# Optimization experiments

Hardware: AMD Instinct MI355X
Metric: run time of the kernel (lower is better)

Reference implementation:

```python
import jax, jax.numpy as jnp
import numpy as np
from math import factorial

N_NODES = 10000
N_EDGES = 320000
FEAT = 32
NBASIS = 8
RMAX = 6.0
ZMAX = 119


def _cg(j1, m1, j2, m2, j3, m3):
    if m1 + m2 != m3 or j3 < abs(j1 - j2) or j3 > j1 + j2:
        return 0.0
    f = lambda n: float(factorial(n))
    pre = ((2 * j3 + 1) * f(j1 + j2 - j3) * f(j1 - j2 + j3) * f(-j1 + j2 + j3) / f(j1 + j2 + j3 + 1)) ** 0.5
    pre *= (f(j3 + m3) * f(j3 - m3) * f(j1 - m1) * f(j1 + m1) * f(j2 - m2) * f(j2 + m2)) ** 0.5
    s = 0.0
    for k in range(j1 + j2 + j3 + 1):
        d = [k, j1 + j2 - j3 - k, j1 - m1 - k, j2 + m2 - k, j3 - j2 + m1 + k, j3 - j1 - m2 + k]
        if min(d) < 0:
            continue
        s += (-1) ** k / (f(d[0]) * f(d[1]) * f(d[2]) * f(d[3]) * f(d[4]) * f(d[5]))
    return pre * s


def _u_real(l):
    # complex->real spherical harmonics unitary transform
    U = np.zeros((2 * l + 1, 2 * l + 1), dtype=complex)
    s2 = 1.0 / np.sqrt(2.0)
    for m in range(-l, l + 1):
        i = m + l
        if m == 0:
            U[i, l] = 1.0
        elif m > 0:
            U[i, l + m] = ((-1) ** m) * s2
            U[i, l - m] = s2
        else:
            U[i, l + m] = 1j * s2
            U[i, l - m] = -1j * ((-1) ** m) * s2
    return U


def _real_cg():
    # real Clebsch-Gordan coupling coefficients for l<=2, shape (9,9,9), sparse
    off = [0, 1, 4]
    C = np.zeros((9, 9, 9))
    Us = [_u_real(l) for l in range(3)]
    for l1 in range(3):
        for l2 in range(3):
            for l3 in range(3):
                if l3 < abs(l1 - l2) or l3 > l1 + l2:
                    continue
                cg = np.zeros((2 * l1 + 1, 2 * l2 + 1, 2 * l3 + 1))
                for m1 in range(-l1, l1 + 1):
                    for m2 in range(-l2, l2 + 1):
                        m3 = m1 + m2
                        if abs(m3) <= l3:
                            cg[m1 + l1, m2 + l2, m3 + l3] = _cg(l1, m1, l2, m2, l3, m3)
                blk = np.einsum('ia,jb,kc,abc->ijk', Us[l1], Us[l2], np.conj(Us[l3]), cg.astype(complex))
                C[off[l1]:off[l1] + 2 * l1 + 1, off[l2]:off[l2] + 2 * l2 + 1, off[l3]:off[l3] + 2 * l3 + 1] = blk.real + blk.imag
    return C

CGC = jnp.asarray(_real_cg(), dtype=jnp.float32)
SL = [slice(0, 1), slice(1, 4), slice(4, 9)]
PATHS0 = [(0, 0, 0), (0, 1, 1), (0, 2, 2)]
PATHS1 = [(l1, l2, l3) for l1 in range(3) for l2 in range(3) for l3 in range(3) if abs(l1 - l2) <= l3 <= l1 + l2]
PATHS2 = [(0, 0, 0), (1, 1, 0), (2, 2, 0)]


def _real_sph(u):
    x, y, z = u[:, 0], u[:, 1], u[:, 2]
    c0 = 0.28209479177387814
    c1 = 0.4886025119029199
    c2a = 1.0925484305920792
    c2b = 0.31539156525252005
    c2c = 0.5462742152960396
    return jnp.stack([c0 * jnp.ones_like(x), c1 * y, c1 * z, c1 * x,
                      c2a * x * y, c2a * y * z, c2b * (3.0 * z * z - 1.0), c2a * x * z,
                      c2c * (x * x - y * y)], axis=-1)


def _message_pass(x, rad, Y, src, dst, W, paths, out_dim, n_nodes):
    # gather src node features -> per-edge CG tensor product with (radial x Ylm) basis -> scatter-add to dst
    xs = x[src, 0]  # (E, Dx, F)
    msg = jnp.zeros((rad.shape[0], out_dim, x.shape[-1]), x.dtype)
    for p, (l1, l2, l3) in enumerate(paths):
        w = rad @ W[p]  # (E, F) learned radial path weights
        contrib = jnp.einsum('abc,eaf,eb,ef->ecf', CGC[SL[l1], SL[l2], SL[l3]], xs[:, SL[l1], :], Y[:, SL[l2]], w)
        msg = msg.at[:, SL[l3], :].add(contrib)
    y = jax.ops.segment_sum(msg, dst, num_segments=n_nodes)
    return y[:, None]  # (N, 1, out_dim, F)


def _eadd(a, b):
    if a.shape[2] == b.shape[2]:
        return a + b
    if a.shape[2] < b.shape[2]:
        a, b = b, a
    return a.at[:, :, :b.shape[2], :].add(b)


def _edense(x, K, b):
    # equivariant Dense: shared kernel across degrees, bias only on scalar (l=0) channel
    y = jnp.einsum('npdf,fg->npdg', x, K)
    return y.at[:, :, 0, :].add(b)


def _esilu(x):
    # silu on scalars, sigmoid(scalar)-gated scaling on l>0 components (equivariant)
    if x.shape[2] == 1:
        return jax.nn.silu(x)
    s = x[:, :, 0:1, :]
    return jnp.concatenate([jax.nn.silu(s), x[:, :, 1:, :] * jax.nn.sigmoid(s)], axis=2)


def _forward(dr_vec, Z, neighbor_idxs, embed, wmp0, wmp1, wmp2, dk1, db1, dk2, db2):
    idx_i, idx_j = neighbor_idxs[0], neighbor_idxs[1]
    nN = Z.shape[0]
    r = jnp.sqrt(jnp.sum(dr_vec * dr_vec, axis=-1) + 1e-12)  # (E,)
    u = dr_vec / r[:, None]
    n = jnp.arange(1, NBASIS + 1, dtype=dr_vec.dtype)
    rad = jnp.sqrt(2.0 / RMAX) * jnp.sin(n * jnp.pi * r[:, None] / RMAX) / r[:, None]  # Bessel radial basis
    t = jnp.clip(r / RMAX, 0.0, 1.0 - 1e-6)
    cut = jnp.where(r < RMAX, jnp.exp(1.0 - 1.0 / (1.0 - t * t)), 0.0)  # smooth cutoff
    mask = (idx_i != idx_j).astype(dr_vec.dtype)  # mask padding/self edges
    rad = rad * (cut * mask)[:, None]
    Y = _real_sph(u)  # (E, 9)
    x = embed[Z][:, None, None, :]  # (N, 1, 1, F)
    for it, (paths, W) in enumerate([(PATHS0, wmp0), (PATHS1, wmp1), (PATHS2, wmp2)]):
        last = it == 2
        y = _message_pass(x, rad, Y, idx_j, idx_i, W, paths, 1 if last else 9, nN)
        if last:
            x = x[:, :, 0:1, :]  # change_max_degree_or_type -> scalars only
        y = _eadd(x, y)
        y = _edense(y, dk1[it], db1[it])
        y = _esilu(y)
        y = _edense(y, dk2[it], db2[it])
        x = _eadd(x, y)
    return x[:, 0, 0, :]


def setup_inputs():
    key = jax.random.key(0)
    ks = jax.random.split(key, 10)
    dr_vec = 2.0 * jax.random.normal(ks[0], (N_EDGES, 3), jnp.float32)
    Z = jax.random.randint(ks[1], (N_NODES,), 0, ZMAX)
    neighbor_idxs = jax.random.randint(ks[2], (2, N_EDGES), 0, N_NODES)
    embed = jax.random.normal(ks[3], (ZMAX, FEAT), jnp.float32)
    sB = 1.0 / np.sqrt(NBASIS)
    wmp0 = sB * jax.random.normal(ks[4], (len(PATHS0), NBASIS, FEAT), jnp.float32)
    wmp1 = sB * jax.random.normal(ks[5], (len(PATHS1), NBASIS, FEAT), jnp.float32)
    wmp2 = sB * jax.random.normal(ks[6], (len(PATHS2), NBASIS, FEAT), jnp.float32)
    sF = 1.0 / np.sqrt(FEAT)
    dense_k1 = sF * jax.random.normal(ks[7], (3, FEAT, FEAT), jnp.float32)
    dense_b1 = jnp.zeros((3, FEAT), jnp.float32)
    dense_k2 = 0.1 * sF * jax.random.normal(ks[8], (3, FEAT, FEAT), jnp.float32)
    dense_b2 = jnp.zeros((3, FEAT), jnp.float32)
    return {"dr_vec": dr_vec, "Z": Z, "neighbor_idxs": neighbor_idxs, "embed": embed,
            "wmp0": wmp0, "wmp1": wmp1, "wmp2": wmp2,
            "dense_k1": dense_k1, "dense_b1": dense_b1, "dense_k2": dense_k2, "dense_b2": dense_b2}


def reference(dr_vec, Z, neighbor_idxs, embed, wmp0, wmp1, wmp2, dense_k1, dense_b1, dense_k2, dense_b2):
    return _forward(dr_vec, Z, neighbor_idxs, embed, wmp0, wmp1, wmp2, dense_k1, dense_b1, dense_k2, dense_b2)
```

## Files before the change

kernel.cpp:

```cpp
#include <hip/hip_runtime.h>
#include <type_traits>
#include <cstdint>
#include <cstddef>

#define N_FEAT 32
#define NBASIS 8
#define SPAN   16
#define BSLOTS 8
#define BEDGES (SPAN*BSLOTS)

namespace cgc {

constexpr double dfact(int n){ double r=1.0; for(int i=2;i<=n;++i) r*=(double)i; return r; }

constexpr double dsqrt(double x){
  if(x<=0.0) return 0.0;
  double g = x>1.0 ? x : 1.0;
  for(int i=0;i<200;++i){ double ng = 0.5*(g + x/g); if(ng==g) break; g=ng; }
  return g;
}

constexpr double cg1(int j1,int m1,int j2,int m2,int j3,int m3){
  int adiff = j1-j2; if(adiff<0) adiff=-adiff;
  if(m1+m2!=m3 || j3<adiff || j3>j1+j2) return 0.0;
  double pre = dsqrt((double)(2*j3+1)*dfact(j1+j2-j3)*dfact(j1-j2+j3)*dfact(-j1+j2+j3)/dfact(j1+j2+j3+1));
  pre = pre*dsqrt(dfact(j3+m3)*dfact(j3-m3)*dfact(j1-m1)*dfact(j1+m1)*dfact(j2-m2)*dfact(j2+m2));
  double s=0.0;
  for(int k=0;k<=j1+j2+j3;++k){
    int d1=j1+j2-j3-k, d2=j1-m1-k, d3=j2+m2-k, d4=j3-j2+m1+k, d5=j3-j1-m2+k;
    if(d1<0||d2<0||d3<0||d4<0||d5<0) continue;
    double term = 1.0/(dfact(k)*dfact(d1)*dfact(d2)*dfact(d3)*dfact(d4)*dfact(d5));
    s += (k&1)? -term : term;
  }
  return pre*s;
}

struct Tab { float v[9][9][9]; };

constexpr Tab make(){
  Tab T{};
  int off[3]={0,1,4};
  double Ure[3][5][5]={}, Uim[3][5][5]={};
  const double s2 = dsqrt(0.5);
  for(int l=0;l<3;++l){
    for(int m=-l;m<=l;++m){
      int i=m+l;
      if(m==0){ Ure[l][i][l]=1.0; }
      else if(m>0){
        Ure[l][i][l+m] = ((m&1)? -1.0:1.0)*s2;
        Ure[l][i][l-m] = s2;
      } else {
        int am=-m;
        Uim[l][i][l+m] = s2;
        Uim[l][i][l-m] = -(((am&1)?-1.0:1.0))*s2;
      }
    }
  }
  for(int l1=0;l1<3;++l1) for(int l2=0;l2<3;++l2) for(int l3=0;l3<3;++l3){
    int lo = l1-l2; if(lo<0) lo=-lo;
    if(l3<lo || l3>l1+l2) continue;
    int d1=2*l1+1, d2=2*l2+1, d3=2*l3+1;
    double cg[5][5][5]={};
    for(int m1=-l1;m1<=l1;++m1) for(int m2=-l2;m2<=l2;++m2){
      int m3=m1+m2;
      if(m3>=-l3 && m3<=l3) cg[m1+l1][m2+l2][m3+l3] = cg1(l1,m1,l2,m2,l3,m3);
    }
    double t1re[5][5][5]={}, t1im[5][5][5]={};
    for(int a=0;a<d1;++a) for(int b=0;b<d2;++b) for(int k=0;k<d3;++k){
      double sre=0, sim=0;
      for(int c=0;c<d3;++c){
        double g=cg[a][b][c]; if(g==0.0) continue;
        sre += g*Ure[l3][k][c];
        sim -= g*Uim[l3][k][c];
      }
      t1re[a][b][k]=sre; t1im[a][b][k]=sim;
    }
    double t2re[5][5][5]={}, t2im[5][5][5]={};
    for(int a=0;a<d1;++a) for(int j=0;j<d2;++j) for(int k=0;k<d3;++k){
      double sre=0,sim=0;
      for(int b=0;b<d2;++b){
        double ur=Ure[l2][j][b], ui=Uim[l2][j][b];
        if(ur==0.0&&ui==0.0) continue;
        sre += ur*t1re[a][b][k]-ui*t1im[a][b][k];
        sim += ur*t1im[a][b][k]+ui*t1re[a][b][k];
      }
      t2re[a][j][k]=sre; t2im[a][j][k]=sim;
    }
    for(int i=0;i<d1;++i) for(int j=0;j<d2;++j) for(int k=0;k<d3;++k){
      double sre=0,sim=0;
      for(int a=0;a<d1;++a){
        double ur=Ure[l1][i][a], ui=Uim[l1][i][a];
        if(ur==0.0&&ui==0.0) continue;
        sre += ur*t2re[a][j][k]-ui*t2im[a][j][k];
        sim += ur*t2im[a][j][k]+ui*t2re[a][j][k];
      }
      T.v[off[l1]+i][off[l2]+j][off[l3]+k] = (float)(sre+sim);
    }
  }
  return T;
}

constexpr Tab T = make();

}

template<int I, int N, typename F>
__device__ __forceinline__ void sfor(F&& f){
  if constexpr (I < N){
    f(std::integral_constant<int,I>{});
    sfor<I+1,N>(static_cast<F&&>(f));
  }
}

constexpr int LOFF[3] = {0,1,4};
constexpr float Y0C = 0.28209479177387814f;

struct PS0 {
  static constexpr int NP=3;
  static constexpr int L[3][3]={{0,0,0},{0,1,1},{0,2,2}};
  static constexpr int ALO=0, AHI=1, OD=9, WOFF=0;
  static constexpr int MINW=4, DEPTH=8;
  static constexpr bool EMB=true;
};
struct PS1a {
  static constexpr int NP=9;
  static constexpr int L[9][3]={{0,0,0},{0,1,1},{0,2,2},
                                {1,0,1},{1,1,0},{1,1,1},{1,1,2},{1,2,1},{1,2,2}};
  static constexpr int ALO=0, AHI=4, OD=9, WOFF=0;
  static constexpr int MINW=3, DEPTH=3;
  static constexpr bool EMB=false;
};
struct PS1b {
  static constexpr int NP=6;
  static constexpr int L[6][3]={{2,0,2},{2,1,1},{2,1,2},{2,2,0},{2,2,1},{2,2,2}};
  static constexpr int ALO=4, AHI=9, OD=9, WOFF=9*NBASIS*N_FEAT;
  static constexpr int MINW=3, DEPTH=3;
  static constexpr bool EMB=false;
};
struct PS2 {
  static constexpr int NP=3;
  static constexpr int L[3][3]={{0,0,0},{1,1,0},{2,2,0}};
  static constexpr int ALO=0, AHI=9, OD=1, WOFF=0;
  static constexpr int MINW=3, DEPTH=5;
  static constexpr bool EMB=false;
};

__global__ void init_kernel(const float* __restrict__ embed, const int* __restrict__ Z,
                            float* __restrict__ xA, float* __restrict__ ymsg,
                            int* __restrict__ cnt, int nN){
  int i = blockIdx.x*256 + threadIdx.x;
  if(i >= nN*N_FEAT) return;
  int n = i>>5, f = i&31;
  if(f==0) cnt[n]=0;
  xA[(size_t)n*288 + f] = embed[Z[n]*N_FEAT + f];
  #pragma unroll
  for(int c=0;c<9;++c) ymsg[((size_t)n*9+c)*32 + f] = 0.f;
}

__global__ void count_kernel(const int* __restrict__ dst, int* __restrict__ cnt, int E){
  int e = blockIdx.x*256 + threadIdx.x;
  if(e<E) atomicAdd(&cnt[dst[e]], 1);
}

__global__ void __launch_bounds__(1024) scan_kernel(const int* __restrict__ cnt,
                                                    int* __restrict__ cursor, int n){
  __shared__ int part[1024];
  const int tid = threadIdx.x;
  const int chunk = (n + 1023) >> 10;
  const int s0 = tid*chunk;
  const int s1 = (s0+chunk < n) ? s0+chunk : n;
  int s=0;
  for(int i=s0;i<s1;++i) s += cnt[i];
  part[tid]=s; __syncthreads();
  for(int off=1; off<1024; off<<=1){
    int v = 0;
    if(tid>=off) v = part[tid-off];
    __syncthreads();
    part[tid] += v;
    __syncthreads();
  }
  int run = part[tid] - s;
  for(int i=s0;i<s1;++i){
    int cv = cnt[i];
    cursor[i]=run;
    run += cv;
  }
}

__global__ void fillgeom_kernel(const int* __restrict__ dst, const int* __restrict__ src,
                                const int* __restrict__ Z, const float* __restrict__ dr,
                                int* __restrict__ cursor, int* __restrict__ srcsP,
                                unsigned char* __restrict__ zsrc,
                                float* __restrict__ radY, int E){
  int e = blockIdx.x*256 + threadIdx.x;
  if(e>=E) return;
  const int d = dst[e], s = src[e];
  const int pos = atomicAdd(&cursor[d], 1);
  srcsP[pos] = s | (d<<16);
  zsrc[pos]  = (unsigned char)Z[s];

  float dx=dr[3*e], dy=dr[3*e+1], dz=dr[3*e+2];
  float r2 = fmaf(dx,dx,fmaf(dy,dy,fmaf(dz,dz,1e-12f)));
  float r = sqrtf(r2);
  float inv = 1.f/r;
  float ux=dx*inv, uy=dy*inv, uz=dz*inv;
  float t = r*(1.f/6.f);
  t = fminf(fmaxf(t,0.f), 1.f-1e-6f);
  float cut = 0.f;
  if (r < 6.f) cut = __expf(1.f - 1.f/(1.f - t*t));
  if (d==s) cut = 0.f;
  float base = 0.57735026918962576f * inv * cut;
  float* o = radY + (size_t)pos*16;
  const float pir = 0.52359877559829887f * r;
  float sT, cT;
  __sincosf(pir, &sT, &cT);
  const float twoc = 2.f*cT;
  float sp = 0.f, sc = sT;
  o[0] = base*sc;
  #pragma unroll
  for(int nb=2; nb<=8; ++nb){
    float sn = fmaf(twoc, sc, -sp);
    o[nb-1] = base*sn;
    sp = sc; sc = sn;
  }
  o[8]  = 0.4886025119029199f*uy;
  o[9]  = 0.4886025119029199f*uz;
  o[10] = 0.4886025119029199f*ux;
  o[11] = 1.0925484305920792f*ux*uy;
  o[12] = 1.0925484305920792f*uy*uz;
  o[13] = 0.31539156525252005f*(3.f*uz*uz-1.f);
  o[14] = 1.0925484305920792f*ux*uz;
  o[15] = 0.5462742152960396f*(ux*ux-uy*uy);
}

template<class PS>
__device__ __forceinline__ void mp_phase(
    int k0, int nE, const float* sRad, const int* sS, const unsigned char* sZb,
    const float* __restrict__ x_in, const float* __restrict__ emb,
    const float* __restrict__ W, float* __restrict__ ymsg, int f)
{
  constexpr int NP = PS::NP;
  constexpr int ALO = PS::ALO, AHI = PS::AHI, DA = AHI-ALO;
  constexpr int OD = PS::OD;
  constexpr int DEPTH = PS::DEPTH, NBUF = DEPTH+1;

  float Wreg[NP][NBASIS];
  sfor<0,NP>([&](auto P){
    constexpr int p = P.value;
    constexpr bool fold = (PS::L[p][1]==0);
    sfor<0,NBASIS>([&](auto Q){
      float v = W[PS::WOFF + (p*NBASIS+Q.value)*N_FEAT + f];
      if constexpr (fold) v *= Y0C;
      Wreg[p][Q.value] = v;
    });
  });

  float msg[OD];
  sfor<0,OD>([&](auto C){ msg[C.value]=0.f; });

  auto gather = [&](float (&dst)[DA], int k){
    if constexpr (PS::EMB){
      const int zs = sZb[k];
      dst[0] = emb[zs*N_FEAT + f];
    } else {
      const int s = sS[k] & 0xFFFF;
      const float* xb = x_in + (size_t)s*288 + ALO*N_FEAT + f;
      sfor<0,DA>([&](auto A){ dst[A.value] = xb[A.value*N_FEAT]; });
    }
  };

  auto compute = [&](const float (&xs)[DA], int k){
    const float* rp = sRad + k*16;
    const float4 q0 = *(const float4*)(rp);
    const float4 q1 = *(const float4*)(rp+4);
    const float4 q2 = *(const float4*)(rp+8);
    const float4 q3 = *(const float4*)(rp+12);
    const float rad[8] = {q0.x,q0.y,q0.z,q0.w,q1.x,q1.y,q1.z,q1.w};
    const float Yv[8]  = {q2.x,q2.y,q2.z,q2.w,q3.x,q3.y,q3.z,q3.w};
    sfor<0,NP>([&](auto P){
      constexpr int p  = P.value;
      constexpr int l1 = PS::L[p][0], l2 = PS::L[p][1], l3 = PS::L[p][2];
      constexpr int o1 = LOFF[l1], o2 = LOFF[l2], o3 = LOFF[l3];
      float w = 0.f;
      sfor<0,NBASIS>([&](auto Q){ w = fmaf(rad[Q.value], Wreg[p][Q.value], w); });
      sfor<0,2*l2+1>([&](auto B){
        constexpr int b = B.value;
        float yw;
        if constexpr (l2==0) yw = w;
        else                 yw = Yv[o2+b-1]*w;
        sfor<0,2*l1+1>([&](auto A){
          constexpr int a = A.value;
          sfor<0,2*l3+1>([&](auto C){
            constexpr int c = C.value;
            constexpr float cgv = cgc::T.v[o1+a][o2+b][o3+c];
            if constexpr (cgv > 1e-7f || cgv < -1e-7f){
              msg[o3+c] = fmaf(cgv*xs[o1+a-ALO], yw, msg[o3+c]);
            }
          });
        });
      });
    });
  };

  auto flush = [&](int d){
    float* yb = ymsg + ((size_t)d*OD)*N_FEAT + f;
    sfor<0,OD>([&](auto C){
      atomicAdd(yb + C.value*N_FEAT, msg[C.value]);
      msg[C.value] = 0.f;
    });
  };

  if (k0 + SPAN <= nE){
    float buf[NBUF][DA];
    sfor<0,DEPTH>([&](auto J){ gather(buf[J.value], k0 + J.value); });
    int vcur = sS[k0];
    sfor<0,SPAN>([&](auto I){
      constexpr int i = I.value;
      int vnext;
      if constexpr (i+1 < SPAN) vnext = sS[k0+i+1]; else vnext = -1;
      if constexpr (i+DEPTH < SPAN) gather(buf[(i+DEPTH)%NBUF], k0+i+DEPTH);
      compute(buf[i%NBUF], k0+i);
      if (i == SPAN-1 || (vnext>>16) != (vcur>>16)) flush(vcur>>16);
      vcur = vnext;
    });
  } else {
    const int k1 = (k0+SPAN < nE) ? k0+SPAN : nE;
    for (int k=k0; k<k1; ++k){
      float xs[DA];
      gather(xs, k);
      compute(xs, k);
      const int dc = sS[k]>>16;
      const int dn = (k+1 < k1) ? (sS[k+1]>>16) : -1;
      if (dn != dc) flush(dc);
    }
  }
}

template<bool EMB>
__device__ __forceinline__ int mp_stage(
    int bid, float* sRad, int* sS, unsigned char* sZb,
    const int* __restrict__ srcsP, const unsigned char* __restrict__ zsrc,
    const float* __restrict__ radY, int E)
{
  const int tid  = threadIdx.x;
  const int base = bid * BEDGES;
  const int nE   = (base + BEDGES <= E) ? BEDGES : (E - base);
  {
    const float4* g4 = (const float4*)(radY + (size_t)base*16);
    float4* s4 = (float4*)sRad;
    const int n4 = nE*4;
    for (int i=tid; i<n4; i+=256) s4[i] = g4[i];
    for (int i=tid; i<nE;  i+=256) sS[i] = srcsP[base+i];
    if constexpr (EMB){
      for (int i=tid; i<nE; i+=256) sZb[i] = zsrc[base+i];
    }
  }
  __syncthreads();
  return nE;
}

template<class PS>
__global__ void __launch_bounds__(256, PS::MINW) mp_kernel(
    const int* __restrict__ srcsP, const unsigned char* __restrict__ zsrc,
    const float* __restrict__ radY, const float* __restrict__ x_in,
    const float* __restrict__ emb, const float* __restrict__ W,
    float* __restrict__ ymsg, int E)
{
  __shared__ float sRad[BEDGES*16];
  __shared__ int   sS[BEDGES];
  __shared__ unsigned char sZb[BEDGES];
  const int nE = mp_stage<PS::EMB>(blockIdx.x, sRad, sS, sZb, srcsP, zsrc, radY, E);
  const int f  = threadIdx.x & 31;
  const int k0 = (threadIdx.x>>5)*SPAN;
  if (k0 >= nE) return;
  mp_phase<PS>(k0, nE, sRad, sS, sZb, x_in, emb, W, ymsg, f);
}

__global__ void __launch_bounds__(256, 3) mp1_kernel(
    const int* __restrict__ srcsP, const float* __restrict__ radY,
    const float* __restrict__ x_in, const float* __restrict__ W,
    float* __restrict__ ymsg, int E, int gMP)
{
  __shared__ float sRad[BEDGES*16];
  __shared__ int   sS[BEDGES];
  const int b = blockIdx.x;
  if (b < gMP){
    const int nE = mp_stage<false>(b, sRad, sS, nullptr, srcsP, nullptr, radY, E);
    const int f  = threadIdx.x & 31;
    const int k0 = (threadIdx.x>>5)*SPAN;
    if (k0 >= nE) return;
    mp_phase<PS1a>(k0, nE, sRad, sS, nullptr, x_in, nullptr, W, ymsg, f);
  } else {
    const int nE = mp_stage<false>(b-gMP, sRad, sS, nullptr, srcsP, nullptr, radY, E);
    const int f  = threadIdx.x & 31;
    const int k0 = (threadIdx.x>>5)*SPAN;
    if (k0 >= nE) return;
    mp_phase<PS1b>(k0, nE, sRad, sS, nullptr, x_in, nullptr, W, ymsg, f);
  }
}

template<int DX, bool ZERO>
__global__ void __launch_bounds__(256) nodeA_kernel(
    const float* __restrict__ xin, float* __restrict__ ymsg,
    float* __restrict__ ymsg2,
    const float* __restrict__ K1, const float* __restrict__ b1,
    const float* __restrict__ K2, const float* __restrict__ b2,
    float* __restrict__ xout, int nN)
{
  __shared__ float sK1[1024], sK2[1024], sb1[32], sb2[32];
  __shared__ float tb[8][9][32];
  const int tid = threadIdx.x;
  for(int i=tid;i<1024;i+=256){ sK1[i]=K1[i]; sK2[i]=K2[i]; }
  if(tid<32){ sb1[tid]=b1[tid]; sb2[tid]=b2[tid]; }
  __syncthreads();
  const int h = tid>>5, f = tid&31;
  const int n = blockIdx.x*8 + h;
  const bool valid = n < nN;
  const int nc = valid ? n : 0;
  float xi[9];
  #pragma unroll
  for(int c=0;c<9;++c){
    float t = ymsg[((size_t)nc*9+c)*32+f];
    if (ZERO && valid) ymsg[((size_t)nc*9+c)*32+f] = 0.f;
    float x = 0.f;
    if (c<DX) x = xin[((size_t)nc*9+c)*32+f];
    xi[c]=x;
    tb[h][c][f] = t + x;
  }
  if (ZERO && valid) ymsg2[(size_t)nc*32+f] = 0.f;
  __syncthreads();
  float u[9];
  #pragma unroll
  for(int c=0;c<9;++c){
    float acc = (c==0) ? sb1[f] : 0.f;
    #pragma unroll
    for(int g=0;g<32;++g) acc = fmaf(tb[h][c][g], sK1[g*32+f], acc);
    u[c]=acc;
  }
  const float gate = 1.f/(1.f+expf(-u[0]));
  __syncthreads();
  #pragma unroll
  for(int c=0;c<9;++c) tb[h][c][f] = u[c]*gate;
  __syncthreads();
  #pragma unroll
  for(int c=0;c<9;++c){
    float acc = (c==0) ? sb2[f] : 0.f;
    #pragma unroll
    for(int g=0;g<32;++g) acc = fmaf(tb[h][c][g], sK2[g*32+f], acc);
    if (valid) xout[((size_t)n*9+c)*32+f] = acc + ((c<DX) ? xi[c] : 0.f);
  }
}

__global__ void __launch_bounds__(256) nodeB_kernel(
    const float* __restrict__ xin, const float* __restrict__ msg0,
    const float* __restrict__ K1, const float* __restrict__ b1,
    const float* __restrict__ K2, const float* __restrict__ b2,
    float* __restrict__ out, int nN)
{
  __shared__ float sK1[1024], sK2[1024], sb1[32], sb2[32];
  __shared__ float tb[8][32];
  const int tid = threadIdx.x;
  for(int i=tid;i<1024;i+=256){ sK1[i]=K1[i]; sK2[i]=K2[i]; }
  if(tid<32){ sb1[tid]=b1[tid]; sb2[tid]=b2[tid]; }
  __syncthreads();
  const int h = tid>>5, f = tid&31;
  const int n = blockIdx.x*8 + h;
  const bool valid = n < nN;
  const int nc = valid ? n : 0;
  const float x0 = xin[(size_t)nc*288 + f];
  tb[h][f] = msg0[(size_t)nc*32+f] + x0;
  __syncthreads();
  float acc = sb1[f];
  #pragma unroll
  for(int g=0;g<32;++g) acc = fmaf(tb[h][g], sK1[g*32+f], acc);
  const float gate = 1.f/(1.f+expf(-acc));
  const float v = acc*gate;
  __syncthreads();
  tb[h][f] = v;
  __syncthreads();
  float acc2 = sb2[f];
  #pragma unroll
  for(int g=0;g<32;++g) acc2 = fmaf(tb[h][g], sK2[g*32+f], acc2);
  if (valid) out[(size_t)n*32+f] = x0 + acc2;
}

extern "C" void kernel_launch(void* const* d_in, const int* in_sizes, int n_in,
                              void* d_out, int out_size, void* d_ws, size_t ws_size,
                              hipStream_t stream) {
  const float* dr    = (const float*)d_in[0];
  const int*   Z     = (const int*)  d_in[1];
  const int*   nbr   = (const int*)  d_in[2];
  const float* embed = (const float*)d_in[3];
  const float* wmp0  = (const float*)d_in[4];
  const float* wmp1  = (const float*)d_in[5];
  const float* wmp2  = (const float*)d_in[6];
  const float* dk1   = (const float*)d_in[7];
  const float* db1   = (const float*)d_in[8];
  const float* dk2   = (const float*)d_in[9];
  const float* db2   = (const float*)d_in[10];
  const int nN = in_sizes[1];
  const int E  = in_sizes[2]/2;
  const int* idx_i = nbr;
  const int* idx_j = nbr + E;

  uintptr_t base = (uintptr_t)d_ws;
  auto alloc = [&](size_t bytes)->void*{
    uintptr_t p = (base + 255) & ~(uintptr_t)255;
    base = p + bytes;
    return (void*)p;
  };
  float* radY    = (float*)alloc((size_t)E*16*4);
  int*   cnt     = (int*)  alloc((size_t)nN*4);
  int*   cursor  = (int*)  alloc((size_t)nN*4);
  int*   srcsP   = (int*)  alloc((size_t)E*4);
  unsigned char* zsrc = (unsigned char*)alloc((size_t)E);
  float* xA      = (float*)alloc((size_t)nN*288*4);
  float* xB      = (float*)alloc((size_t)nN*288*4);
  float* ymsg    = (float*)alloc((size_t)nN*288*4);
  float* ymsg2   = (float*)alloc((size_t)nN*32*4);

  const int gE  = (E+255)/256;
  const int gI  = (nN*N_FEAT+255)/256;
  const int gND = (nN+7)/8;
  const int gMP = (E + BEDGES - 1) / BEDGES;

  init_kernel    <<<gI, 256, 0, stream>>>(embed, Z, xA, ymsg, cnt, nN);
  count_kernel   <<<gE, 256, 0, stream>>>(idx_i, cnt, E);
  scan_kernel    <<<1, 1024, 0, stream>>>(cnt, cursor, nN);
  fillgeom_kernel<<<gE, 256, 0, stream>>>(idx_i, idx_j, Z, dr, cursor, srcsP, zsrc, radY, E);

  mp_kernel<PS0><<<gMP, 256, 0, stream>>>(srcsP, zsrc, radY, xA, embed, wmp0, ymsg, E);
  nodeA_kernel<1,true><<<gND, 256, 0, stream>>>(xA, ymsg, ymsg2, dk1, db1, dk2, db2, xB, nN);
  mp1_kernel<<<2*gMP, 256, 0, stream>>>(srcsP, radY, xB, wmp1, ymsg, E, gMP);
  nodeA_kernel<9,false><<<gND, 256, 0, stream>>>(xB, ymsg, ymsg2, dk1+1024, db1+32, dk2+1024, db2+32, xA, nN);
  mp_kernel<PS2><<<gMP, 256, 0, stream>>>(srcsP, zsrc, radY, xA, embed, wmp2, ymsg2, E);
  nodeB_kernel<<<gND, 256, 0, stream>>>(xA, ymsg2, dk1+2048, db1+64, dk2+2048, db2+64,
                                        (float*)d_out, nN);
}
```

Before: 399.4 us.

## Drop edges outside the cutoff radius and self-loops before message passing

```diff
diff --git a/kernel.cpp b/kernel.cpp
--- a/kernel.cpp
+++ b/kernel.cpp
@@ -145,6 +145,15 @@
   static constexpr bool EMB=false;
 };
 
+__device__ __forceinline__ bool edge_live(const float* __restrict__ dr, int e,
+                                          int d, int s, float& r_out){
+  float dx=dr[3*e], dy=dr[3*e+1], dz=dr[3*e+2];
+  float r2 = fmaf(dx,dx,fmaf(dy,dy,fmaf(dz,dz,1e-12f)));
+  float r = sqrtf(r2);
+  r_out = r;
+  return (r < 6.f) && (d != s);
+}
+
 __global__ void init_kernel(const float* __restrict__ embed, const int* __restrict__ Z,
                             float* __restrict__ xA, float* __restrict__ ymsg,
                             int* __restrict__ cnt, int nN){
@@ -157,13 +166,18 @@
   for(int c=0;c<9;++c) ymsg[((size_t)n*9+c)*32 + f] = 0.f;
 }
 
-__global__ void count_kernel(const int* __restrict__ dst, int* __restrict__ cnt, int E){
+__global__ void count_kernel(const int* __restrict__ dst, const int* __restrict__ src,
+                             const float* __restrict__ dr, int* __restrict__ cnt, int E){
   int e = blockIdx.x*256 + threadIdx.x;
-  if(e<E) atomicAdd(&cnt[dst[e]], 1);
+  if(e>=E) return;
+  const int d = dst[e], s = src[e];
+  float r;
+  if (edge_live(dr, e, d, s, r)) atomicAdd(&cnt[d], 1);
 }
 
 __global__ void __launch_bounds__(1024) scan_kernel(const int* __restrict__ cnt,
-                                                    int* __restrict__ cursor, int n){
+                                                    int* __restrict__ cursor,
+                                                    int* __restrict__ Elive, int n){
   __shared__ int part[1024];
   const int tid = threadIdx.x;
   const int chunk = (n + 1023) >> 10;
@@ -185,6 +199,7 @@
     cursor[i]=run;
     run += cv;
   }
+  if(tid==1023) Elive[0] = run;
 }
 
 __global__ void fillgeom_kernel(const int* __restrict__ dst, const int* __restrict__ src,
@@ -195,20 +210,18 @@
   int e = blockIdx.x*256 + threadIdx.x;
   if(e>=E) return;
   const int d = dst[e], s = src[e];
+  float r;
+  if (!edge_live(dr, e, d, s, r)) return;
   const int pos = atomicAdd(&cursor[d], 1);
   srcsP[pos] = s | (d<<16);
   zsrc[pos]  = (unsigned char)Z[s];
 
   float dx=dr[3*e], dy=dr[3*e+1], dz=dr[3*e+2];
-  float r2 = fmaf(dx,dx,fmaf(dy,dy,fmaf(dz,dz,1e-12f)));
-  float r = sqrtf(r2);
   float inv = 1.f/r;
   float ux=dx*inv, uy=dy*inv, uz=dz*inv;
   float t = r*(1.f/6.f);
   t = fminf(fmaxf(t,0.f), 1.f-1e-6f);
-  float cut = 0.f;
-  if (r < 6.f) cut = __expf(1.f - 1.f/(1.f - t*t));
-  if (d==s) cut = 0.f;
+  const float cut = __expf(1.f - 1.f/(1.f - t*t));
   float base = 0.57735026918962576f * inv * cut;
   float* o = radY + (size_t)pos*16;
   const float pir = 0.52359877559829887f * r;
@@ -364,11 +377,12 @@
     const int* __restrict__ srcsP, const unsigned char* __restrict__ zsrc,
     const float* __restrict__ radY, const float* __restrict__ x_in,
     const float* __restrict__ emb, const float* __restrict__ W,
-    float* __restrict__ ymsg, int E)
+    float* __restrict__ ymsg, const int* __restrict__ Elive)
 {
   __shared__ float sRad[BEDGES*16];
   __shared__ int   sS[BEDGES];
   __shared__ unsigned char sZb[BEDGES];
+  const int E = Elive[0];
   const int nE = mp_stage<PS::EMB>(blockIdx.x, sRad, sS, sZb, srcsP, zsrc, radY, E);
   const int f  = threadIdx.x & 31;
   const int k0 = (threadIdx.x>>5)*SPAN;
@@ -379,10 +393,11 @@
 __global__ void __launch_bounds__(256, 3) mp1_kernel(
     const int* __restrict__ srcsP, const float* __restrict__ radY,
     const float* __restrict__ x_in, const float* __restrict__ W,
-    float* __restrict__ ymsg, int E, int gMP)
+    float* __restrict__ ymsg, const int* __restrict__ Elive, int gMP)
 {
   __shared__ float sRad[BEDGES*16];
   __shared__ int   sS[BEDGES];
+  const int E = Elive[0];
   const int b = blockIdx.x;
   if (b < gMP){
     const int nE = mp_stage<false>(b, sRad, sS, nullptr, srcsP, nullptr, radY, E);
@@ -512,6 +527,7 @@
   float* radY    = (float*)alloc((size_t)E*16*4);
   int*   cnt     = (int*)  alloc((size_t)nN*4);
   int*   cursor  = (int*)  alloc((size_t)nN*4);
+  int*   Elive   = (int*)  alloc(256);
   int*   srcsP   = (int*)  alloc((size_t)E*4);
   unsigned char* zsrc = (unsigned char*)alloc((size_t)E);
   float* xA      = (float*)alloc((size_t)nN*288*4);
@@ -525,15 +541,15 @@
   const int gMP = (E + BEDGES - 1) / BEDGES;
 
   init_kernel    <<<gI, 256, 0, stream>>>(embed, Z, xA, ymsg, cnt, nN);
-  count_kernel   <<<gE, 256, 0, stream>>>(idx_i, cnt, E);
-  scan_kernel    <<<1, 1024, 0, stream>>>(cnt, cursor, nN);
+  count_kernel   <<<gE, 256, 0, stream>>>(idx_i, idx_j, dr, cnt, E);
+  scan_kernel    <<<1, 1024, 0, stream>>>(cnt, cursor, Elive, nN);
   fillgeom_kernel<<<gE, 256, 0, stream>>>(idx_i, idx_j, Z, dr, cursor, srcsP, zsrc, radY, E);
 
-  mp_kernel<PS0><<<gMP, 256, 0, stream>>>(srcsP, zsrc, radY, xA, embed, wmp0, ymsg, E);
+  mp_kernel<PS0><<<gMP, 256, 0, stream>>>(srcsP, zsrc, radY, xA, embed, wmp0, ymsg, Elive);
   nodeA_kernel<1,true><<<gND, 256, 0, stream>>>(xA, ymsg, ymsg2, dk1, db1, dk2, db2, xB, nN);
-  mp1_kernel<<<2*gMP, 256, 0, stream>>>(srcsP, radY, xB, wmp1, ymsg, E, gMP);
+  mp1_kernel<<<2*gMP, 256, 0, stream>>>(srcsP, radY, xB, wmp1, ymsg, Elive, gMP);
   nodeA_kernel<9,false><<<gND, 256, 0, stream>>>(xB, ymsg, ymsg2, dk1+1024, db1+32, dk2+1024, db2+32, xA, nN);
-  mp_kernel<PS2><<<gMP, 256, 0, stream>>>(srcsP, zsrc, radY, xA, embed, wmp2, ymsg2, E);
+  mp_kernel<PS2><<<gMP, 256, 0, stream>>>(srcsP, zsrc, radY, xA, embed, wmp2, ymsg2, Elive);
   nodeB_kernel<<<gND, 256, 0, stream>>>(xA, ymsg2, dk1+2048, db1+64, dk2+2048, db2+64,
                                         (float*)d_out, nN);
 }
```

Result: no change. 394.6 us (median of 2 runs) (-1.2%).
